# Optimization experiments

Measured on AMD Instinct MI355X. Metric: run time of the kernel, lower is better.

## Reference

```python
import jax, jax.numpy as jnp
import numpy as np

EPS = 1e-5

def _h_swish(y):
    # x * relu6(x+3)/6
    return y * jnp.clip(y + 3.0, 0.0, 6.0) / 6.0

def setup_inputs() -> dict:
    key = jax.random.key(0)
    ks = jax.random.split(key, 12)
    n, c, h, w = 16, 256, 64, 64
    inp = oup = c
    mip = max(8, inp // 32)  # groups=32 -> mip=8
    return {
        "x": jax.random.normal(ks[0], (n, c, h, w), jnp.float32),
        "residual": jax.random.normal(ks[1], (n, c, h, w), jnp.float32),
        "w1": jax.random.normal(ks[2], (mip, inp), jnp.float32) * 0.05,
        "b1": jax.random.normal(ks[3], (mip,), jnp.float32) * 0.05,
        "bn_gamma": jnp.ones((mip,), jnp.float32),
        "bn_beta": jnp.zeros((mip,), jnp.float32),
        "bn_mean": jax.random.normal(ks[4], (mip,), jnp.float32) * 0.05,
        "bn_var": jax.random.uniform(ks[5], (mip,), jnp.float32, 0.5, 1.5),
        "w2": jax.random.normal(ks[6], (oup, mip), jnp.float32) * 0.05,
        "b2": jax.random.normal(ks[7], (oup,), jnp.float32) * 0.05,
        "w3": jax.random.normal(ks[8], (oup, mip), jnp.float32) * 0.05,
        "b3": jax.random.normal(ks[9], (oup,), jnp.float32) * 0.05,
    }

def reference(x, residual, w1, b1, bn_gamma, bn_beta, bn_mean, bn_var, w2, b2, w3, b3):
    n, c, h, w = x.shape
    # bilinear resize of residual to x's spatial size (align_corners=False)
    res_r = jax.image.resize(residual, x.shape, method="linear")
    xs = x + res_r  # [n,c,h,w]
    # directional average pools
    x_h = xs.mean(axis=3, keepdims=True)                      # [n,c,h,1]
    x_w = xs.mean(axis=2, keepdims=True).transpose(0, 1, 3, 2)  # [n,c,w,1]
    y = jnp.concatenate([x_h, x_w], axis=2)                   # [n,c,h+w,1]
    # 1x1 conv -> BN (inference) -> h_swish
    y = jnp.einsum("nchw,mc->nmhw", y, w1) + b1[None, :, None, None]
    inv = bn_gamma / jnp.sqrt(bn_var + EPS)
    y = (y - bn_mean[None, :, None, None]) * inv[None, :, None, None] + bn_beta[None, :, None, None]
    y = _h_swish(y)                                           # [n,mip,h+w,1]
    yh, yw = y[:, :, :h, :], y[:, :, h:, :]                   # [n,mip,h,1],[n,mip,w,1]
    yw = yw.transpose(0, 1, 3, 2)                             # [n,mip,1,w]
    a_h = jax.nn.sigmoid(jnp.einsum("nmhw,om->nohw", yh, w2) + b2[None, :, None, None])  # [n,c,h,1]
    a_w = jax.nn.sigmoid(jnp.einsum("nmhw,om->nohw", yw, w3) + b3[None, :, None, None])  # [n,c,1,w]
    wei = a_h * a_w                                           # [n,c,h,w] via broadcast
    return 2.0 * xs * wei + 2.0 * residual * (1.0 - wei)
```

## Files before the change

### kernel.cpp

```cpp
#include <hip/hip_runtime.h>
#include <math.h>

#define NB 16
#define CB 256
#define MIP 8
#define EPSV 1e-5f

__global__ __launch_bounds__(256) void k_reduce(const float* __restrict__ x,
                                                const float* __restrict__ res,
                                                float* __restrict__ xh,
                                                float* __restrict__ xw) {
    int bid = blockIdx.x;
    int plane = (bid & 7) + 8 * (511 - (bid >> 3));
    const float4* px4 = (const float4*)(x   + (size_t)plane * 4096);
    const float4* pr4 = (const float4*)(res + (size_t)plane * 4096);
    __shared__ float spad[256];
    int t = threadIdx.x;

    float4 a[4], b[4];
#pragma unroll
    for (int i = 0; i < 4; i++) a[i] = px4[i * 256 + t];
#pragma unroll
    for (int i = 0; i < 4; i++) b[i] = pr4[i * 256 + t];

    float csum0 = 0.f, csum1 = 0.f, csum2 = 0.f, csum3 = 0.f;
    float rsum[4];
#pragma unroll
    for (int i = 0; i < 4; i++) {
        float s0 = a[i].x + b[i].x, s1 = a[i].y + b[i].y;
        float s2 = a[i].z + b[i].z, s3 = a[i].w + b[i].w;
        csum0 += s0; csum1 += s1; csum2 += s2; csum3 += s3;
        rsum[i] = (s0 + s1) + (s2 + s3);
    }

#pragma unroll
    for (int i = 0; i < 4; i++) {
        float rs = rsum[i];
        rs += __shfl_xor(rs, 1);
        rs += __shfl_xor(rs, 2);
        rs += __shfl_xor(rs, 4);
        rs += __shfl_xor(rs, 8);
        rsum[i] = rs;
    }
    if ((t & 15) == 0) {
        int g = t >> 4;
#pragma unroll
        for (int i = 0; i < 4; i++)
            xh[(size_t)plane * 64 + i * 16 + g] = rsum[i] * 0.015625f;
    }

    csum0 += __shfl_xor(csum0, 16); csum0 += __shfl_xor(csum0, 32);
    csum1 += __shfl_xor(csum1, 16); csum1 += __shfl_xor(csum1, 32);
    csum2 += __shfl_xor(csum2, 16); csum2 += __shfl_xor(csum2, 32);
    csum3 += __shfl_xor(csum3, 16); csum3 += __shfl_xor(csum3, 32);
    int wv = t >> 6;
    int j  = t & 15;
    if ((t & 63) < 16) {
        float* d = &spad[wv * 64 + j * 4];
        d[0] = csum0; d[1] = csum1; d[2] = csum2; d[3] = csum3;
    }
    __syncthreads();
    if (t < 64)
        xw[(size_t)plane * 64 + t] =
            (spad[t] + spad[64 + t] + spad[128 + t] + spad[192 + t]) * 0.015625f;
}

__global__ __launch_bounds__(256) void k_mid_a(const float* __restrict__ xh,
                                               const float* __restrict__ xw,
                                               const float* __restrict__ w1,
                                               const float* __restrict__ b1,
                                               const float* __restrict__ gamma,
                                               const float* __restrict__ beta,
                                               const float* __restrict__ mean,
                                               const float* __restrict__ var,
                                               float* __restrict__ yl) {
    int n = blockIdx.x;
    int t = threadIdx.x;
    int p  = t & 127;
    int mg = (t >> 7) * 4;
    const float* pool = (p < 64) ? (xh + (size_t)n * CB * 64 + p)
                                 : (xw + (size_t)n * CB * 64 + (p - 64));
    float acc[4] = {0.f, 0.f, 0.f, 0.f};
    for (int c = 0; c < CB; c++) {
        float pv = pool[(size_t)c * 64];
#pragma unroll
        for (int k = 0; k < 4; k++) acc[k] += pv * w1[(mg + k) * CB + c];
    }
#pragma unroll
    for (int k = 0; k < 4; k++) {
        int m = mg + k;
        float yv = acc[k] + b1[m];
        float inv = gamma[m] * rsqrtf(var[m] + EPSV);
        yv = (yv - mean[m]) * inv + beta[m];
        float cl = fminf(fmaxf(yv + 3.f, 0.f), 6.f);
        yl[((size_t)n * MIP + m) * 128 + p] = yv * cl * (1.f / 6.f);
    }
}

__global__ __launch_bounds__(256) void k_apply(const float* __restrict__ x,
                                               const float* __restrict__ res,
                                               const float* __restrict__ yl,
                                               const float* __restrict__ w2,
                                               const float* __restrict__ b2,
                                               const float* __restrict__ w3,
                                               const float* __restrict__ b3,
                                               float* __restrict__ out) {
    int plane = blockIdx.x;
    int n = plane >> 8;
    int o = plane & 255;
    const float4* px4 = (const float4*)(x   + (size_t)plane * 4096);
    const float4* pr4 = (const float4*)(res + (size_t)plane * 4096);
    float4*       po4 = (float4*)(out + (size_t)plane * 4096);
    __shared__ float sah[64], saw[64];
    int t = threadIdx.x;
    if (t < 128) {
        int hh  = t & 63;
        int off = (t < 64) ? 0 : 64;
        const float* wv = (t < 64) ? (w2 + o * MIP) : (w3 + o * MIP);
        float acc = (t < 64) ? b2[o] : b3[o];
        const float* ylp = yl + (size_t)n * MIP * 128 + off + hh;
#pragma unroll
        for (int m = 0; m < MIP; m++) acc += ylp[m * 128] * wv[m];
        float sig = 1.f / (1.f + __expf(-acc));
        if (t < 64) sah[hh] = sig; else saw[hh] = sig;
    }
    __syncthreads();
    const float4 sw4 = *(const float4*)&saw[4 * (t & 15)];
#pragma unroll
    for (int i = 0; i < 4; i++) {
        int row = i * 16 + (t >> 4);
        float ahr2 = 2.f * sah[row];
        float4 a = px4[i * 256 + t];
        float4 b = pr4[i * 256 + t];
        float4 oo;
        oo.x = a.x * (ahr2 * sw4.x) + 2.f * b.x;
        oo.y = a.y * (ahr2 * sw4.y) + 2.f * b.y;
        oo.z = a.z * (ahr2 * sw4.z) + 2.f * b.z;
        oo.w = a.w * (ahr2 * sw4.w) + 2.f * b.w;
        po4[i * 256 + t] = oo;
    }
}

extern "C" void kernel_launch(void* const* d_in, const int* in_sizes, int n_in,
                              void* d_out, int out_size, void* d_ws, size_t ws_size,
                              hipStream_t stream) {
    const float* x     = (const float*)d_in[0];
    const float* res   = (const float*)d_in[1];
    const float* w1    = (const float*)d_in[2];
    const float* b1    = (const float*)d_in[3];
    const float* gamma = (const float*)d_in[4];
    const float* beta  = (const float*)d_in[5];
    const float* mean  = (const float*)d_in[6];
    const float* var   = (const float*)d_in[7];
    const float* w2    = (const float*)d_in[8];
    const float* b2    = (const float*)d_in[9];
    const float* w3    = (const float*)d_in[10];
    const float* b3    = (const float*)d_in[11];
    float* out = (float*)d_out;

    float* ws = (float*)d_ws;
    float* xh = ws;
    float* xw = ws + 262144;
    float* yl = ws + 524288;

    k_reduce<<<NB * CB, 256, 0, stream>>>(x, res, xh, xw);
    k_mid_a<<<NB, 256, 0, stream>>>(xh, xw, w1, b1, gamma, beta, mean, var, yl);
    k_apply<<<NB * CB, 256, 0, stream>>>(x, res, yl, w2, b2, w3, b3, out);
}
```

Before: 71.23 us.

## Parallelize mid stage and precompute attention maps before the apply kernel

The middle kernel grows from one block per batch to eight blocks per batch. Each block splits the 256-channel reduction across two halves and combines them in shared memory. The same kernel now also runs the second 1x1 convs and the sigmoid, writing the per-plane h and w attention vectors to workspace. The apply kernel then just loads the 128 precomputed values per plane instead of redoing an 8-tap matvec and exp in each of 4096 blocks. This trades a serial, low-occupancy middle kernel and redundant apply-side work for extra workspace writes and reads.

```diff
diff --git a/kernel.cpp b/kernel.cpp
--- a/kernel.cpp
+++ b/kernel.cpp
@@ -32,7 +32,6 @@
         csum0 += s0; csum1 += s1; csum2 += s2; csum3 += s3;
         rsum[i] = (s0 + s1) + (s2 + s3);
     }
-
 #pragma unroll
     for (int i = 0; i < 4; i++) {
         float rs = rsum[i];
@@ -48,7 +47,6 @@
         for (int i = 0; i < 4; i++)
             xh[(size_t)plane * 64 + i * 16 + g] = rsum[i] * 0.015625f;
     }
-
     csum0 += __shfl_xor(csum0, 16); csum0 += __shfl_xor(csum0, 32);
     csum1 += __shfl_xor(csum1, 16); csum1 += __shfl_xor(csum1, 32);
     csum2 += __shfl_xor(csum2, 16); csum2 += __shfl_xor(csum2, 32);
@@ -65,65 +63,78 @@
             (spad[t] + spad[64 + t] + spad[128 + t] + spad[192 + t]) * 0.015625f;
 }
 
-__global__ __launch_bounds__(256) void k_mid_a(const float* __restrict__ xh,
-                                               const float* __restrict__ xw,
-                                               const float* __restrict__ w1,
-                                               const float* __restrict__ b1,
-                                               const float* __restrict__ gamma,
-                                               const float* __restrict__ beta,
-                                               const float* __restrict__ mean,
-                                               const float* __restrict__ var,
-                                               float* __restrict__ yl) {
-    int n = blockIdx.x;
-    int t = threadIdx.x;
-    int p  = t & 127;
-    int mg = (t >> 7) * 4;
-    const float* pool = (p < 64) ? (xh + (size_t)n * CB * 64 + p)
-                                 : (xw + (size_t)n * CB * 64 + (p - 64));
-    float acc[4] = {0.f, 0.f, 0.f, 0.f};
-    for (int c = 0; c < CB; c++) {
-        float pv = pool[(size_t)c * 64];
+__global__ __launch_bounds__(256) void k_mid(const float* __restrict__ xh,
+                                             const float* __restrict__ xw,
+                                             const float* __restrict__ w1,
+                                             const float* __restrict__ b1,
+                                             const float* __restrict__ gamma,
+                                             const float* __restrict__ beta,
+                                             const float* __restrict__ mean,
+                                             const float* __restrict__ var,
+                                             const float* __restrict__ w2,
+                                             const float* __restrict__ b2,
+                                             const float* __restrict__ w3,
+                                             const float* __restrict__ b3,
+                                             float* __restrict__ ah,
+                                             float* __restrict__ aw) {
+    int n  = blockIdx.x >> 3;
+    int pc = blockIdx.x & 7;
+    int t  = threadIdx.x;
+    int ph = t & 15;
+    int p  = pc * 16 + ph;
+    int m  = (t >> 4) & 7;
+    int half = t >> 7;
+    __shared__ float part[256];
+    __shared__ float ylds[MIP * 16];
+
+    const float* pool = (p < 64) ? (xh + ((size_t)n * CB) * 64 + p)
+                                 : (xw + ((size_t)n * CB) * 64 + (p - 64));
+    float acc = 0.f;
+    int c0 = half * 128;
+#pragma unroll 16
+    for (int ci = 0; ci < 128; ci++) {
+        int c = c0 + ci;
+        acc += pool[(size_t)c * 64] * w1[m * CB + c];
+    }
+    part[t] = acc;
+    __syncthreads();
+    if (t < 128) {
+        float val = part[t] + part[t + 128] + b1[m];
+        float inv = gamma[m] * rsqrtf(var[m] + EPSV);
+        val = (val - mean[m]) * inv + beta[m];
+        float cl = fminf(fmaxf(val + 3.f, 0.f), 6.f);
+        ylds[m * 16 + ph] = val * cl * (1.f / 6.f);
+    }
+    __syncthreads();
+
+    const float* wsel = (p < 64) ? w2 : w3;
+    const float* bsel = (p < 64) ? b2 : b3;
+    float* osel = (p < 64) ? (ah + ((size_t)n * CB) * 64 + p)
+                           : (aw + ((size_t)n * CB) * 64 + (p - 64));
 #pragma unroll
-        for (int k = 0; k < 4; k++) acc[k] += pv * w1[(mg + k) * CB + c];
-    }
+    for (int oo = 0; oo < 16; oo++) {
+        int o = oo * 16 + (t >> 4);
+        float acc2 = bsel[o];
 #pragma unroll
-    for (int k = 0; k < 4; k++) {
-        int m = mg + k;
-        float yv = acc[k] + b1[m];
-        float inv = gamma[m] * rsqrtf(var[m] + EPSV);
-        yv = (yv - mean[m]) * inv + beta[m];
-        float cl = fminf(fmaxf(yv + 3.f, 0.f), 6.f);
-        yl[((size_t)n * MIP + m) * 128 + p] = yv * cl * (1.f / 6.f);
+        for (int mm = 0; mm < MIP; mm++)
+            acc2 += wsel[o * MIP + mm] * ylds[mm * 16 + ph];
+        osel[(size_t)o * 64] = 1.f / (1.f + __expf(-acc2));
     }
 }
 
 __global__ __launch_bounds__(256) void k_apply(const float* __restrict__ x,
                                                const float* __restrict__ res,
-                                               const float* __restrict__ yl,
-                                               const float* __restrict__ w2,
-                                               const float* __restrict__ b2,
-                                               const float* __restrict__ w3,
-                                               const float* __restrict__ b3,
+                                               const float* __restrict__ ah,
+                                               const float* __restrict__ aw,
                                                float* __restrict__ out) {
     int plane = blockIdx.x;
-    int n = plane >> 8;
-    int o = plane & 255;
     const float4* px4 = (const float4*)(x   + (size_t)plane * 4096);
     const float4* pr4 = (const float4*)(res + (size_t)plane * 4096);
     float4*       po4 = (float4*)(out + (size_t)plane * 4096);
     __shared__ float sah[64], saw[64];
     int t = threadIdx.x;
-    if (t < 128) {
-        int hh  = t & 63;
-        int off = (t < 64) ? 0 : 64;
-        const float* wv = (t < 64) ? (w2 + o * MIP) : (w3 + o * MIP);
-        float acc = (t < 64) ? b2[o] : b3[o];
-        const float* ylp = yl + (size_t)n * MIP * 128 + off + hh;
-#pragma unroll
-        for (int m = 0; m < MIP; m++) acc += ylp[m * 128] * wv[m];
-        float sig = 1.f / (1.f + __expf(-acc));
-        if (t < 64) sah[hh] = sig; else saw[hh] = sig;
-    }
+    if (t < 64)       sah[t]      = ah[(size_t)plane * 64 + t];
+    else if (t < 128) saw[t - 64] = aw[(size_t)plane * 64 + (t - 64)];
     __syncthreads();
     const float4 sw4 = *(const float4*)&saw[4 * (t & 15)];
 #pragma unroll
@@ -161,9 +172,11 @@
     float* ws = (float*)d_ws;
     float* xh = ws;
     float* xw = ws + 262144;
-    float* yl = ws + 524288;
+    float* ah = ws + 524288;
+    float* aw = ws + 786432;
 
     k_reduce<<<NB * CB, 256, 0, stream>>>(x, res, xh, xw);
-    k_mid_a<<<NB, 256, 0, stream>>>(xh, xw, w1, b1, gamma, beta, mean, var, yl);
-    k_apply<<<NB * CB, 256, 0, stream>>>(x, res, yl, w2, b2, w3, b3, out);
+    k_mid<<<NB * 8, 256, 0, stream>>>(xh, xw, w1, b1, gamma, beta, mean, var,
+                                      w2, b2, w3, b3, ah, aw);
+    k_apply<<<NB * CB, 256, 0, stream>>>(x, res, ah, aw, out);
 }
```

Result: faster. 57.34 us (median of 2 runs) (-19.5%).
